# Performance work log

Hardware: AMD Instinct MI355X
Metric: run time of the kernel (lower is better)

Reference implementation:

```python
import jax, jax.numpy as jnp
import numpy as np
from jax import lax

MU = 255
H = 64            # block_hidden_size
SKIP = 256        # skip_size
NUM_LAYERS = 24
CYCLE = 6
UP_CONV = 4       # upsample_convs=[4]
UP_REPEAT = 75
LF = 80           # local_features_size
B = 2
L = 64            # local feature frames
T = L * UP_CONV * UP_REPEAT  # 19200 signal samples


def setup_inputs() -> dict:
    key = jax.random.key(0)
    ks = jax.random.split(key, 16)
    r = lambda k, shape, sc=0.05: jax.random.normal(k, shape, jnp.float32) * sc
    return {
        "local_features": jax.random.normal(ks[0], (B, L, LF), jnp.float32),
        "gold_signal": jax.random.uniform(ks[1], (B, T), jnp.float32, minval=-1.0, maxval=1.0),
        "embed_w": r(ks[2], (H, 1)),
        "embed_b": r(ks[3], (H,)),
        "up_w": r(ks[4], (LF, LF, UP_CONV)),
        "up_b": r(ks[5], (LF,)),
        "proj_w": r(ks[6], (NUM_LAYERS * 2 * H, LF)),
        "proj_b": r(ks[7], (NUM_LAYERS * 2 * H,)),
        "dil_w": r(ks[8], (NUM_LAYERS, 2 * H, H, 2)),
        "dil_b": r(ks[9], (NUM_LAYERS, 2 * H)),
        "skip_w": r(ks[10], (NUM_LAYERS, SKIP, H)),
        "skip_b": r(ks[11], (NUM_LAYERS, SKIP)),
        "res_w": r(ks[12], (NUM_LAYERS - 1, H, H)),
        "res_b": r(ks[13], (NUM_LAYERS - 1, H)),
        "out1_w": r(ks[14], (MU + 1, SKIP)),
        "out2_w": r(ks[15], (MU + 1, MU + 1)),
    }


def _causal_dilated_conv(x, w, b, dilation):
    # x: [B, C, T]; w: [O, C, 2]; left-pad so output[t] depends on inputs <= t
    xp = jnp.pad(x, ((0, 0), (0, 0), (dilation, 0)))
    y = lax.conv_general_dilated(xp, w, window_strides=(1,), padding="VALID",
                                 rhs_dilation=(dilation,),
                                 dimension_numbers=("NCH", "OIH", "NCH"))
    return y + b[None, :, None]


def _upsample(local_features, up_w, up_b, proj_w, proj_b):
    # local_features: [B, L, LF] -> cond [B, NUM_LAYERS, 2H, T]
    x = jnp.transpose(local_features, (0, 2, 1))  # [B, LF, L]
    # ConvTranspose1d with kernel_size == stride == UP_CONV (no overlap)
    y = jnp.einsum("bfl,fgk->bglk", x, up_w).reshape(x.shape[0], LF, -1)
    y = y + up_b[None, :, None]                                  # [B, LF, L*4]
    # 1x1 projection to per-layer gate conditioning (chunking in the original
    # is a memory trick, math-identical to a single conv)
    z = jnp.einsum("bft,of->bot", y, proj_w) + proj_b[None, :, None]
    z = jnp.repeat(z, UP_REPEAT, axis=-1)                        # [B, NL*2H, T]
    return z.reshape(z.shape[0], NUM_LAYERS, 2 * H, -1)


def reference(local_features, gold_signal, embed_w, embed_b, up_w, up_b,
              proj_w, proj_b, dil_w, dil_b, skip_w, skip_b, res_w, res_b,
              out1_w, out2_w):
    cond = _upsample(local_features, up_w, up_b, proj_w, proj_b)
    # embed: Conv1d(1 -> H, kernel 1)
    x = gold_signal[:, None, :] * embed_w[None, :, :] + embed_b[None, :, None]
    skip_sum = None
    for i in range(NUM_LAYERS):
        dilation = 2 ** (i % CYCLE)
        y = _causal_dilated_conv(x, dil_w[i], dil_b[i], dilation) + cond[:, i]
        gated = jnp.tanh(y[:, :H]) * jax.nn.sigmoid(y[:, H:])
        skip = jnp.einsum("bht,sh->bst", gated, skip_w[i]) + skip_b[i][None, :, None]
        skip_sum = skip if skip_sum is None else skip_sum + skip
        if i < NUM_LAYERS - 1:  # last layer has no residual out_conv
            x = x + jnp.einsum("bht,oh->bot", gated, res_w[i]) + res_b[i][None, :, None]
    h = jnp.einsum("bst,os->bot", jax.nn.relu(skip_sum), out1_w)
    h = jnp.einsum("bst,os->bot", jax.nn.relu(h), out2_w)
    return jax.nn.log_softmax(h, axis=1)  # [B, MU+1, T]
```

## Files before the change

kernel.cpp:

```cpp
#include <hip/hip_runtime.h>
#include <math.h>

#define T_TOT 19200
#define HD    64
#define SKIPN 256
#define NLAYER 24
#define LFN   80
#define NB    2
#define NTL   128
#define HALO  64
#define XR    (NTL + HALO)
#define NGT   (T_TOT / NTL)
#define NOH   64
#define NTH   (T_TOT / NOH)

typedef float  f32x4  __attribute__((ext_vector_type(4)));
typedef __bf16 bf16x8 __attribute__((ext_vector_type(8)));
typedef __bf16 bf16x4 __attribute__((ext_vector_type(4)));

__device__ __forceinline__ f32x4 mfma16(bf16x8 a, bf16x8 b, f32x4 c) {
    return __builtin_amdgcn_mfma_f32_16x16x32_bf16(a, b, c, 0, 0, 0);
}

__global__ __launch_bounds__(256) void prep_kernel(
    const float* __restrict__ dil_w, const float* __restrict__ skip_w,
    const float* __restrict__ skip_b, const float* __restrict__ res_w,
    const float* __restrict__ out1_w, const float* __restrict__ out2_w,
    __bf16* __restrict__ A1f, __bf16* __restrict__ Asf, __bf16* __restrict__ A3f,
    __bf16* __restrict__ Ao1f, __bf16* __restrict__ Ao2f, float* __restrict__ sbsum)
{
    int idx = blockIdx.x * 256 + threadIdx.x;
    if (idx < 24 * 128 * 128) {
        {
            int j = idx & 7, lane = (idx >> 3) & 63, ks = (idx >> 9) & 3;
            int mt = (idx >> 11) & 7, l = idx >> 14;
            int row = mt * 16 + (lane & 15);
            int k   = ks * 32 + (lane >> 4) * 8 + j;
            A1f[idx] = (__bf16)dil_w[((l * 128 + row) * 64 + (k & 63)) * 2 + (k >> 6)];
        }
        {
            int j = idx & 7, lane = (idx >> 3) & 63, ks = (idx >> 9) & 1;
            int mt = (idx >> 10) & 15, l = idx >> 14;
            int row = mt * 16 + (lane & 15);
            int k   = ks * 32 + (lane >> 4) * 8 + j;
            Asf[idx] = (__bf16)skip_w[(l * 256 + row) * 64 + k];
        }
    }
    if (idx < 23 * 64 * 64) {
        int j = idx & 7, lane = (idx >> 3) & 63, ks = (idx >> 9) & 1;
        int mt = (idx >> 10) & 3, l = idx >> 12;
        int row = mt * 16 + (lane & 15);
        int k   = ks * 32 + (lane >> 4) * 8 + j;
        A3f[idx] = (__bf16)res_w[(l * 64 + row) * 64 + k];
    }
    if (idx < 256 * 256) {
        int j = idx & 7, lane = (idx >> 3) & 63, ks = (idx >> 9) & 7;
        int mt = idx >> 12;
        int row = mt * 16 + (lane & 15);
        int k   = ks * 32 + (lane >> 4) * 8 + j;
        Ao1f[idx] = (__bf16)out1_w[row * 256 + k];
        Ao2f[idx] = (__bf16)out2_w[row * 256 + k];
    }
    if (idx < 256) {
        float s = 0.0f;
        #pragma unroll
        for (int l = 0; l < NLAYER; ++l) s += skip_b[l * 256 + idx];
        sbsum[idx] = s;
    }
}

__global__ __launch_bounds__(256) void up_kernel(
    const float* __restrict__ lf, const float* __restrict__ up_w,
    const float* __restrict__ up_b, float* __restrict__ y_up)
{
    int idx = blockIdx.x * 256 + threadIdx.x;
    if (idx >= NB * LFN * 256) return;
    int t4 = idx & 255;
    int g  = (idx >> 8) % LFN;
    int b  = idx / (LFN * 256);
    int l = t4 >> 2, k = t4 & 3;
    float acc = up_b[g];
    const float* lfp = lf + (b * 64 + l) * LFN;
    #pragma unroll 8
    for (int f = 0; f < LFN; ++f)
        acc += lfp[f] * up_w[(f * LFN + g) * 4 + k];
    y_up[idx] = acc;
}

__global__ __launch_bounds__(256) void proj_kernel(
    const float* __restrict__ y_up, const float* __restrict__ proj_w,
    const float* __restrict__ proj_b, float* __restrict__ z)
{
    int idx = blockIdx.x * 256 + threadIdx.x;
    if (idx >= NB * 3072 * 256) return;
    int t4 = idx & 255;
    int o  = (idx >> 8) % 3072;
    int b  = idx / (3072 * 256);
    float acc = proj_b[o];
    const float* yp = y_up + b * LFN * 256 + t4;
    const float* wp = proj_w + o * LFN;
    #pragma unroll 8
    for (int g = 0; g < LFN; ++g)
        acc += wp[g] * yp[g * 256];
    z[idx] = acc;
}

__global__ __launch_bounds__(256, 2) void layer_group(
    const float* __restrict__ gold, const float* __restrict__ ew,
    const float* __restrict__ eb,
    const __bf16* __restrict__ xg_in, __bf16* __restrict__ xg_out,
    const float* __restrict__ zbuf, const float* __restrict__ dil_b,
    const float* __restrict__ res_b,
    const __bf16* __restrict__ A1f, const __bf16* __restrict__ A3f,
    __bf16* __restrict__ G, int L0, int first, int last)
{
    __shared__ __bf16 xh[XR][72];
    __shared__ __bf16 Gs[XR][72];
    __shared__ float  zs[4][128];

    const int b    = blockIdx.y;
    const int t0   = blockIdx.x * NTL;
    const int tid  = threadIdx.x;
    const int lane = tid & 63;
    const int w    = tid >> 6;
    const int n16  = lane & 15;
    const int quad = lane >> 4;
    const int q0   = ((t0 - HALO > 0) ? t0 - HALO : 0) / 75;

    bf16x8 z8;
    #pragma unroll
    for (int u = 0; u < 8; ++u) z8[u] = (__bf16)0.0f;

    if (first) {
        for (int idx = tid; idx < XR * 8; idx += 256) {
            int r = idx >> 3, hc = (idx & 7) * 8;
            int t = t0 - HALO + r;
            bf16x8 v = z8;
            if (t >= 0) {
                float gv = gold[b * T_TOT + t];
                #pragma unroll
                for (int u = 0; u < 8; ++u)
                    v[u] = (__bf16)(gv * ew[hc + u] + eb[hc + u]);
            }
            *(bf16x8*)&xh[r][hc] = v;
        }
    } else {
        for (int idx = tid; idx < XR * 8; idx += 256) {
            int r = idx >> 3, hc = (idx & 7) * 8;
            int t = t0 - HALO + r;
            bf16x8 v = (t >= 0)
                ? *(const bf16x8*)&xg_in[((size_t)b * T_TOT + t) * 64 + hc] : z8;
            *(bf16x8*)&xh[r][hc] = v;
        }
    }

    const bf16x8* A1v = (const bf16x8*)A1f;
    const bf16x8* A3v = (const bf16x8*)A3f;
    f32x4 zero4 = {0.0f, 0.0f, 0.0f, 0.0f};

    for (int j = 0; j < 6; ++j) {
        const int l = L0 + j;
        const int d = 1 << j;

        for (int idx = tid; idx < 512; idx += 256) {
            int qq = idx >> 7, o = idx & 127;
            int q = q0 + qq; if (q > 255) q = 255;
            zs[qq][o] = dil_b[l * 128 + o] +
                        zbuf[((size_t)(b * 3072 + l * 128 + o)) * 256 + q];
        }
        bf16x8 a1a[4], a1b[4];
        #pragma unroll
        for (int ks = 0; ks < 4; ++ks) {
            a1a[ks] = A1v[((l * 8 + w) * 4 + ks) * 64 + lane];
            a1b[ks] = A1v[((l * 8 + 4 + w) * 4 + ks) * 64 + lane];
        }
        __syncthreads();

        #pragma unroll
        for (int nt = 0; nt < 12; ++nt) {
            int nn = nt * 16 + n16;
            int rm = (nn >= d) ? nn - d : 0;
            bf16x8 b0 = *(const bf16x8*)&xh[rm][quad * 8];
            bf16x8 b1 = *(const bf16x8*)&xh[rm][32 + quad * 8];
            bf16x8 b2 = *(const bf16x8*)&xh[nn][quad * 8];
            bf16x8 b3 = *(const bf16x8*)&xh[nn][32 + quad * 8];
            f32x4 aa = zero4, ab = zero4;
            aa = mfma16(a1a[0], b0, aa); ab = mfma16(a1b[0], b0, ab);
            aa = mfma16(a1a[1], b1, aa); ab = mfma16(a1b[1], b1, ab);
            aa = mfma16(a1a[2], b2, aa); ab = mfma16(a1b[2], b2, ab);
            aa = mfma16(a1a[3], b3, aa); ab = mfma16(a1b[3], b3, ab);

            int tt = t0 - HALO + nn;
            int qq = ((tt > 0) ? tt : 0) / 75 - q0;
            bf16x4 g4;
            #pragma unroll
            for (int r = 0; r < 4; ++r) {
                int o = w * 16 + quad * 4 + r;
                float ya = aa[r] + zs[qq][o];
                float yb = ab[r] + zs[qq][o + 64];
                float th = 1.0f - 2.0f * __builtin_amdgcn_rcpf(__expf(2.0f * ya) + 1.0f);
                float sg = __builtin_amdgcn_rcpf(1.0f + __expf(-yb));
                g4[r] = (__bf16)(th * sg);
            }
            *(bf16x4*)&Gs[nn][w * 16 + quad * 4] = g4;
        }
        __syncthreads();

        __bf16* Gl = G + (((size_t)l * NB + b) * T_TOT + t0) * 64;
        for (int idx = tid; idx < 128 * 8; idx += 256) {
            int rr = idx >> 3, hc = (idx & 7) * 8;
            *(bf16x8*)&Gl[rr * 64 + hc] = *(const bf16x8*)&Gs[HALO + rr][hc];
        }

        if (l < NLAYER - 1) {
            bf16x8 a3[2];
            #pragma unroll
            for (int ks = 0; ks < 2; ++ks)
                a3[ks] = A3v[((l * 4 + w) * 2 + ks) * 64 + lane];
            int o0 = w * 16 + quad * 4;
            f32x4 rb = *(const f32x4*)&res_b[l * 64 + o0];
            #pragma unroll
            for (int nt = 0; nt < 12; ++nt) {
                int nn = nt * 16 + n16;
                bf16x8 g0 = *(const bf16x8*)&Gs[nn][quad * 8];
                bf16x8 g1 = *(const bf16x8*)&Gs[nn][32 + quad * 8];
                f32x4 ar = zero4;
                ar = mfma16(a3[0], g0, ar);
                ar = mfma16(a3[1], g1, ar);
                bf16x4 xo = *(const bf16x4*)&xh[nn][o0];
                bf16x4 xn;
                #pragma unroll
                for (int r = 0; r < 4; ++r)
                    xn[r] = (__bf16)((float)xo[r] + ar[r] + rb[r]);
                *(bf16x4*)&xh[nn][o0] = xn;
            }
        }
    }

    if (!last) {
        __syncthreads();
        for (int idx = tid; idx < 128 * 8; idx += 256) {
            int rr = idx >> 3, hc = (idx & 7) * 8;
            *(bf16x8*)&xg_out[((size_t)b * T_TOT + t0 + rr) * 64 + hc] =
                *(const bf16x8*)&xh[HALO + rr][hc];
        }
    }
}

__global__ __launch_bounds__(256, 4) void head_mfma(
    const __bf16* __restrict__ G, const __bf16* __restrict__ Asf,
    const float* __restrict__ sbsum, const __bf16* __restrict__ Ao1f,
    const __bf16* __restrict__ Ao2f, float* __restrict__ out)
{
    __shared__ __bf16 Vs[NOH][264];
    __shared__ float redm[4][4][16];
    __shared__ float reds[4][4][16];

    const int b    = blockIdx.y;
    const int t0   = blockIdx.x * NOH;
    const int tid  = threadIdx.x;
    const int lane = tid & 63;
    const int w    = tid >> 6;
    const int n16  = lane & 15;
    const int quad = lane >> 4;

    f32x4 zero4 = {0.0f, 0.0f, 0.0f, 0.0f};
    f32x4 acc[4][4];
    #pragma unroll
    for (int mt = 0; mt < 4; ++mt)
        #pragma unroll
        for (int nt = 0; nt < 4; ++nt) acc[mt][nt] = zero4;

    const bf16x8* Asv = (const bf16x8*)Asf;

    for (int l = 0; l < NLAYER; ++l) {
        const __bf16* Gl = G + (((size_t)l * NB + b) * T_TOT + t0) * 64;
        #pragma unroll
        for (int ks = 0; ks < 2; ++ks) {
            bf16x8 bfr[4];
            #pragma unroll
            for (int nt = 0; nt < 4; ++nt)
                bfr[nt] = *(const bf16x8*)&Gl[(nt * 16 + n16) * 64 + ks * 32 + quad * 8];
            #pragma unroll
            for (int mt = 0; mt < 4; ++mt) {
                bf16x8 af = Asv[((l * 16 + w * 4 + mt) * 2 + ks) * 64 + lane];
                #pragma unroll
                for (int nt = 0; nt < 4; ++nt)
                    acc[mt][nt] = mfma16(af, bfr[nt], acc[mt][nt]);
            }
        }
    }
    {
        int s0 = w * 64 + quad * 4;
        #pragma unroll
        for (int mt = 0; mt < 4; ++mt) {
            #pragma unroll
            for (int nt = 0; nt < 4; ++nt) {
                bf16x4 v4;
                #pragma unroll
                for (int r = 0; r < 4; ++r)
                    v4[r] = (__bf16)fmaxf(acc[mt][nt][r] + sbsum[s0 + mt * 16 + r], 0.0f);
                *(bf16x4*)&Vs[nt * 16 + n16][s0 + mt * 16] = v4;
            }
        }
    }
    __syncthreads();

    const bf16x8* W1v = (const bf16x8*)Ao1f;
    const bf16x8* W2v = (const bf16x8*)Ao2f;

    #pragma unroll
    for (int mt = 0; mt < 4; ++mt)
        #pragma unroll
        for (int nt = 0; nt < 4; ++nt) acc[mt][nt] = zero4;
    #pragma unroll
    for (int ks = 0; ks < 8; ++ks) {
        bf16x8 bfr[4];
        #pragma unroll
        for (int nt = 0; nt < 4; ++nt)
            bfr[nt] = *(const bf16x8*)&Vs[nt * 16 + n16][ks * 32 + quad * 8];
        #pragma unroll
        for (int mt = 0; mt < 4; ++mt) {
            bf16x8 af = W1v[((w * 4 + mt) * 8 + ks) * 64 + lane];
            #pragma unroll
            for (int nt = 0; nt < 4; ++nt)
                acc[mt][nt] = mfma16(af, bfr[nt], acc[mt][nt]);
        }
    }
    __syncthreads();
    #pragma unroll
    for (int mt = 0; mt < 4; ++mt)
        #pragma unroll
        for (int nt = 0; nt < 4; ++nt) {
            int o0 = w * 64 + mt * 16 + quad * 4;
            bf16x4 v4;
            #pragma unroll
            for (int r = 0; r < 4; ++r)
                v4[r] = (__bf16)fmaxf(acc[mt][nt][r], 0.0f);
            *(bf16x4*)&Vs[nt * 16 + n16][o0] = v4;
        }
    __syncthreads();

    #pragma unroll
    for (int mt = 0; mt < 4; ++mt)
        #pragma unroll
        for (int nt = 0; nt < 4; ++nt) acc[mt][nt] = zero4;
    #pragma unroll
    for (int ks = 0; ks < 8; ++ks) {
        bf16x8 bfr[4];
        #pragma unroll
        for (int nt = 0; nt < 4; ++nt)
            bfr[nt] = *(const bf16x8*)&Vs[nt * 16 + n16][ks * 32 + quad * 8];
        #pragma unroll
        for (int mt = 0; mt < 4; ++mt) {
            bf16x8 af = W2v[((w * 4 + mt) * 8 + ks) * 64 + lane];
            #pragma unroll
            for (int nt = 0; nt < 4; ++nt)
                acc[mt][nt] = mfma16(af, bfr[nt], acc[mt][nt]);
        }
    }

    float lmax[4], lsum[4];
    #pragma unroll
    for (int nt = 0; nt < 4; ++nt) {
        float m = -1e30f;
        #pragma unroll
        for (int mt = 0; mt < 4; ++mt)
            #pragma unroll
            for (int r = 0; r < 4; ++r) m = fmaxf(m, acc[mt][nt][r]);
        m = fmaxf(m, __shfl_xor(m, 16, 64));
        m = fmaxf(m, __shfl_xor(m, 32, 64));
        lmax[nt] = m;
    }
    if (quad == 0) {
        #pragma unroll
        for (int nt = 0; nt < 4; ++nt) redm[w][nt][n16] = lmax[nt];
    }
    __syncthreads();
    #pragma unroll
    for (int nt = 0; nt < 4; ++nt) {
        float m = redm[0][nt][n16];
        m = fmaxf(m, redm[1][nt][n16]);
        m = fmaxf(m, redm[2][nt][n16]);
        m = fmaxf(m, redm[3][nt][n16]);
        lmax[nt] = m;
        float s = 0.0f;
        #pragma unroll
        for (int mt = 0; mt < 4; ++mt)
            #pragma unroll
            for (int r = 0; r < 4; ++r) s += __expf(acc[mt][nt][r] - m);
        s += __shfl_xor(s, 16, 64);
        s += __shfl_xor(s, 32, 64);
        lsum[nt] = s;
    }
    if (quad == 0) {
        #pragma unroll
        for (int nt = 0; nt < 4; ++nt) reds[w][nt][n16] = lsum[nt];
    }
    __syncthreads();
    #pragma unroll
    for (int nt = 0; nt < 4; ++nt) {
        float s = reds[0][nt][n16] + reds[1][nt][n16] +
                  reds[2][nt][n16] + reds[3][nt][n16];
        float lse = lmax[nt] + logf(s);
        int t = t0 + nt * 16 + n16;
        #pragma unroll
        for (int mt = 0; mt < 4; ++mt)
            #pragma unroll
            for (int r = 0; r < 4; ++r) {
                int o = w * 64 + mt * 16 + quad * 4 + r;
                out[((size_t)(b * SKIPN + o)) * T_TOT + t] = acc[mt][nt][r] - lse;
            }
    }
}

extern "C" void kernel_launch(void* const* d_in, const int* in_sizes, int n_in,
                              void* d_out, int out_size, void* d_ws, size_t ws_size,
                              hipStream_t stream) {
    const float* lf       = (const float*)d_in[0];
    const float* gold     = (const float*)d_in[1];
    const float* embed_w  = (const float*)d_in[2];
    const float* embed_b  = (const float*)d_in[3];
    const float* up_w     = (const float*)d_in[4];
    const float* up_b     = (const float*)d_in[5];
    const float* proj_w   = (const float*)d_in[6];
    const float* proj_b   = (const float*)d_in[7];
    const float* dil_w    = (const float*)d_in[8];
    const float* dil_b    = (const float*)d_in[9];
    const float* skip_w   = (const float*)d_in[10];
    const float* skip_b   = (const float*)d_in[11];
    const float* res_w    = (const float*)d_in[12];
    const float* res_b    = (const float*)d_in[13];
    const float* out1_w   = (const float*)d_in[14];
    const float* out2_w   = (const float*)d_in[15];

    __bf16* A1f  = (__bf16*)d_ws;
    __bf16* Asf  = A1f + 393216;
    __bf16* A3f  = Asf + 393216;
    __bf16* Ao1f = A3f + 94208;
    __bf16* Ao2f = Ao1f + 65536;
    __bf16* G    = Ao2f + 65536;
    __bf16* xga  = G + (size_t)NLAYER * NB * T_TOT * HD;
    __bf16* xgb  = xga + (size_t)NB * T_TOT * HD;
    float*  sbsum = (float*)(xgb + (size_t)NB * T_TOT * HD);
    float*  y_up  = sbsum + 256;
    float*  zbuf  = y_up + NB * LFN * 256;

    prep_kernel<<<(24 * 128 * 128 + 255) / 256, 256, 0, stream>>>(
        dil_w, skip_w, skip_b, res_w, out1_w, out2_w,
        A1f, Asf, A3f, Ao1f, Ao2f, sbsum);
    up_kernel  <<<(NB * LFN * 256 + 255) / 256, 256, 0, stream>>>(lf, up_w, up_b, y_up);
    proj_kernel<<<(NB * 3072 * 256) / 256,      256, 0, stream>>>(y_up, proj_w, proj_b, zbuf);

    const __bf16* xin[4] = { xga, xga, xgb, xga };
    __bf16*       xout[4] = { xga, xgb, xga, xgb };
    for (int g = 0; g < 4; ++g) {
        layer_group<<<dim3(NGT, NB), 256, 0, stream>>>(
            gold, embed_w, embed_b, xin[g], xout[g],
            zbuf, dil_b, res_b, A1f, A3f, G,
            6 * g, (g == 0) ? 1 : 0, (g == 3) ? 1 : 0);
    }

    head_mfma<<<dim3(NTH, NB), 256, 0, stream>>>(G, Asf, sbsum, Ao1f, Ao2f, (float*)d_out);
}
```

Measured before the change: 408.3 us.

## Double layer_group waves, chunk G layout per time tile, halve head tile

The layer kernel now runs 512 threads per block, with two wave groups each covering half of the 12 time subtiles, which doubles parallelism over the 300 blocks. The gated activation buffer G is relaid out so that each 32-sample chunk holds all 24 layers contiguously, which gives the head kernel locality across layers. The head kernel's time tile shrinks from 64 to 32 samples, doubling its grid for better CU occupancy at the cost of reloading the weights twice as often. Register pressure under launch_bounds(512,4) may force spills.

New measurement: 382.5 us. -6.3%, faster.

```diff
diff --git a/kernel.cpp b/kernel.cpp
--- a/kernel.cpp
+++ b/kernel.cpp
@@ -11,8 +11,9 @@
 #define HALO  64
 #define XR    (NTL + HALO)
 #define NGT   (T_TOT / NTL)
-#define NOH   64
+#define NOH   32
 #define NTH   (T_TOT / NOH)
+#define NCH   (T_TOT / 32)
 
 typedef float  f32x4  __attribute__((ext_vector_type(4)));
 typedef __bf16 bf16x8 __attribute__((ext_vector_type(8)));
@@ -105,7 +106,7 @@
     z[idx] = acc;
 }
 
-__global__ __launch_bounds__(256, 2) void layer_group(
+__global__ __launch_bounds__(512, 4) void layer_group(
     const float* __restrict__ gold, const float* __restrict__ ew,
     const float* __restrict__ eb,
     const __bf16* __restrict__ xg_in, __bf16* __restrict__ xg_out,
@@ -119,10 +120,13 @@
     __shared__ float  zs[4][128];
 
     const int b    = blockIdx.y;
-    const int t0   = blockIdx.x * NTL;
+    const int tb   = blockIdx.x;
+    const int t0   = tb * NTL;
     const int tid  = threadIdx.x;
     const int lane = tid & 63;
     const int w    = tid >> 6;
+    const int wm   = w & 3;
+    const int wg   = w >> 2;
     const int n16  = lane & 15;
     const int quad = lane >> 4;
     const int q0   = ((t0 - HALO > 0) ? t0 - HALO : 0) / 75;
@@ -132,7 +136,7 @@
     for (int u = 0; u < 8; ++u) z8[u] = (__bf16)0.0f;
 
     if (first) {
-        for (int idx = tid; idx < XR * 8; idx += 256) {
+        for (int idx = tid; idx < XR * 8; idx += 512) {
             int r = idx >> 3, hc = (idx & 7) * 8;
             int t = t0 - HALO + r;
             bf16x8 v = z8;
@@ -145,7 +149,7 @@
             *(bf16x8*)&xh[r][hc] = v;
         }
     } else {
-        for (int idx = tid; idx < XR * 8; idx += 256) {
+        for (int idx = tid; idx < XR * 8; idx += 512) {
             int r = idx >> 3, hc = (idx & 7) * 8;
             int t = t0 - HALO + r;
             bf16x8 v = (t >= 0)
@@ -162,8 +166,8 @@
         const int l = L0 + j;
         const int d = 1 << j;
 
-        for (int idx = tid; idx < 512; idx += 256) {
-            int qq = idx >> 7, o = idx & 127;
+        if (tid < 512) {
+            int qq = tid >> 7, o = tid & 127;
             int q = q0 + qq; if (q > 255) q = 255;
             zs[qq][o] = dil_b[l * 128 + o] +
                         zbuf[((size_t)(b * 3072 + l * 128 + o)) * 256 + q];
@@ -171,13 +175,14 @@
         bf16x8 a1a[4], a1b[4];
         #pragma unroll
         for (int ks = 0; ks < 4; ++ks) {
-            a1a[ks] = A1v[((l * 8 + w) * 4 + ks) * 64 + lane];
-            a1b[ks] = A1v[((l * 8 + 4 + w) * 4 + ks) * 64 + lane];
+            a1a[ks] = A1v[((l * 8 + wm) * 4 + ks) * 64 + lane];
+            a1b[ks] = A1v[((l * 8 + 4 + wm) * 4 + ks) * 64 + lane];
         }
         __syncthreads();
 
         #pragma unroll
-        for (int nt = 0; nt < 12; ++nt) {
+        for (int nt0 = 0; nt0 < 6; ++nt0) {
+            int nt = wg * 6 + nt0;
             int nn = nt * 16 + n16;
             int rm = (nn >= d) ? nn - d : 0;
             bf16x8 b0 = *(const bf16x8*)&xh[rm][quad * 8];
@@ -195,33 +200,36 @@
             bf16x4 g4;
             #pragma unroll
             for (int r = 0; r < 4; ++r) {
-                int o = w * 16 + quad * 4 + r;
+                int o = wm * 16 + quad * 4 + r;
                 float ya = aa[r] + zs[qq][o];
                 float yb = ab[r] + zs[qq][o + 64];
                 float th = 1.0f - 2.0f * __builtin_amdgcn_rcpf(__expf(2.0f * ya) + 1.0f);
                 float sg = __builtin_amdgcn_rcpf(1.0f + __expf(-yb));
                 g4[r] = (__bf16)(th * sg);
             }
-            *(bf16x4*)&Gs[nn][w * 16 + quad * 4] = g4;
+            *(bf16x4*)&Gs[nn][wm * 16 + quad * 4] = g4;
         }
         __syncthreads();
 
-        __bf16* Gl = G + (((size_t)l * NB + b) * T_TOT + t0) * 64;
-        for (int idx = tid; idx < 128 * 8; idx += 256) {
-            int rr = idx >> 3, hc = (idx & 7) * 8;
-            *(bf16x8*)&Gl[rr * 64 + hc] = *(const bf16x8*)&Gs[HALO + rr][hc];
+        {
+            __bf16* Gl = G + (((size_t)(b * NCH + tb * 4)) * NLAYER + l) * 2048;
+            for (int idx = tid; idx < 128 * 8; idx += 512) {
+                int rr = idx >> 3, hc = (idx & 7) * 8;
+                size_t off = (size_t)(rr >> 5) * (NLAYER * 2048) + (rr & 31) * 64 + hc;
+                *(bf16x8*)&Gl[off] = *(const bf16x8*)&Gs[HALO + rr][hc];
+            }
         }
 
         if (l < NLAYER - 1) {
             bf16x8 a3[2];
             #pragma unroll
             for (int ks = 0; ks < 2; ++ks)
-                a3[ks] = A3v[((l * 4 + w) * 2 + ks) * 64 + lane];
-            int o0 = w * 16 + quad * 4;
+                a3[ks] = A3v[((l * 4 + wm) * 2 + ks) * 64 + lane];
+            int o0 = wm * 16 + quad * 4;
             f32x4 rb = *(const f32x4*)&res_b[l * 64 + o0];
             #pragma unroll
-            for (int nt = 0; nt < 12; ++nt) {
-                int nn = nt * 16 + n16;
+            for (int nt0 = 0; nt0 < 6; ++nt0) {
+                int nn = (wg * 6 + nt0) * 16 + n16;
                 bf16x8 g0 = *(const bf16x8*)&Gs[nn][quad * 8];
                 bf16x8 g1 = *(const bf16x8*)&Gs[nn][32 + quad * 8];
                 f32x4 ar = zero4;
@@ -239,7 +247,7 @@
 
     if (!last) {
         __syncthreads();
-        for (int idx = tid; idx < 128 * 8; idx += 256) {
+        for (int idx = tid; idx < 128 * 8; idx += 512) {
             int rr = idx >> 3, hc = (idx & 7) * 8;
             *(bf16x8*)&xg_out[((size_t)b * T_TOT + t0 + rr) * 64 + hc] =
                 *(const bf16x8*)&xh[HALO + rr][hc];
@@ -253,11 +261,12 @@
     const __bf16* __restrict__ Ao2f, float* __restrict__ out)
 {
     __shared__ __bf16 Vs[NOH][264];
-    __shared__ float redm[4][4][16];
-    __shared__ float reds[4][4][16];
+    __shared__ float redm[4][2][16];
+    __shared__ float reds[4][2][16];
 
     const int b    = blockIdx.y;
-    const int t0   = blockIdx.x * NOH;
+    const int tcb  = blockIdx.x;
+    const int t0   = tcb * NOH;
     const int tid  = threadIdx.x;
     const int lane = tid & 63;
     const int w    = tid >> 6;
@@ -265,27 +274,28 @@
     const int quad = lane >> 4;
 
     f32x4 zero4 = {0.0f, 0.0f, 0.0f, 0.0f};
-    f32x4 acc[4][4];
+    f32x4 acc[4][2];
     #pragma unroll
     for (int mt = 0; mt < 4; ++mt)
         #pragma unroll
-        for (int nt = 0; nt < 4; ++nt) acc[mt][nt] = zero4;
+        for (int nt = 0; nt < 2; ++nt) acc[mt][nt] = zero4;
 
     const bf16x8* Asv = (const bf16x8*)Asf;
+    const __bf16* Gc  = G + ((size_t)(b * NCH + tcb)) * (NLAYER * 2048);
 
     for (int l = 0; l < NLAYER; ++l) {
-        const __bf16* Gl = G + (((size_t)l * NB + b) * T_TOT + t0) * 64;
+        const __bf16* Gl = Gc + l * 2048;
         #pragma unroll
         for (int ks = 0; ks < 2; ++ks) {
-            bf16x8 bfr[4];
-            #pragma unroll
-            for (int nt = 0; nt < 4; ++nt)
+            bf16x8 bfr[2];
+            #pragma unroll
+            for (int nt = 0; nt < 2; ++nt)
                 bfr[nt] = *(const bf16x8*)&Gl[(nt * 16 + n16) * 64 + ks * 32 + quad * 8];
             #pragma unroll
             for (int mt = 0; mt < 4; ++mt) {
                 bf16x8 af = Asv[((l * 16 + w * 4 + mt) * 2 + ks) * 64 + lane];
                 #pragma unroll
-                for (int nt = 0; nt < 4; ++nt)
+                for (int nt = 0; nt < 2; ++nt)
                     acc[mt][nt] = mfma16(af, bfr[nt], acc[mt][nt]);
             }
         }
@@ -293,16 +303,15 @@
     {
         int s0 = w * 64 + quad * 4;
         #pragma unroll
-        for (int mt = 0; mt < 4; ++mt) {
-            #pragma unroll
-            for (int nt = 0; nt < 4; ++nt) {
+        for (int mt = 0; mt < 4; ++mt)
+            #pragma unroll
+            for (int nt = 0; nt < 2; ++nt) {
                 bf16x4 v4;
                 #pragma unroll
                 for (int r = 0; r < 4; ++r)
                     v4[r] = (__bf16)fmaxf(acc[mt][nt][r] + sbsum[s0 + mt * 16 + r], 0.0f);
                 *(bf16x4*)&Vs[nt * 16 + n16][s0 + mt * 16] = v4;
             }
-        }
     }
     __syncthreads();
 
@@ -312,18 +321,18 @@
     #pragma unroll
     for (int mt = 0; mt < 4; ++mt)
         #pragma unroll
-        for (int nt = 0; nt < 4; ++nt) acc[mt][nt] = zero4;
+        for (int nt = 0; nt < 2; ++nt) acc[mt][nt] = zero4;
     #pragma unroll
     for (int ks = 0; ks < 8; ++ks) {
-        bf16x8 bfr[4];
-        #pragma unroll
-        for (int nt = 0; nt < 4; ++nt)
+        bf16x8 bfr[2];
+        #pragma unroll
+        for (int nt = 0; nt < 2; ++nt)
             bfr[nt] = *(const bf16x8*)&Vs[nt * 16 + n16][ks * 32 + quad * 8];
         #pragma unroll
         for (int mt = 0; mt < 4; ++mt) {
             bf16x8 af = W1v[((w * 4 + mt) * 8 + ks) * 64 + lane];
             #pragma unroll
-            for (int nt = 0; nt < 4; ++nt)
+            for (int nt = 0; nt < 2; ++nt)
                 acc[mt][nt] = mfma16(af, bfr[nt], acc[mt][nt]);
         }
     }
@@ -331,7 +340,7 @@
     #pragma unroll
     for (int mt = 0; mt < 4; ++mt)
         #pragma unroll
-        for (int nt = 0; nt < 4; ++nt) {
+        for (int nt = 0; nt < 2; ++nt) {
             int o0 = w * 64 + mt * 16 + quad * 4;
             bf16x4 v4;
             #pragma unroll
@@ -344,25 +353,25 @@
     #pragma unroll
     for (int mt = 0; mt < 4; ++mt)
         #pragma unroll
-        for (int nt = 0; nt < 4; ++nt) acc[mt][nt] = zero4;
+        for (int nt = 0; nt < 2; ++nt) acc[mt][nt] = zero4;
     #pragma unroll
     for (int ks = 0; ks < 8; ++ks) {
-        bf16x8 bfr[4];
-        #pragma unroll
-        for (int nt = 0; nt < 4; ++nt)
+        bf16x8 bfr[2];
+        #pragma unroll
+        for (int nt = 0; nt < 2; ++nt)
             bfr[nt] = *(const bf16x8*)&Vs[nt * 16 + n16][ks * 32 + quad * 8];
         #pragma unroll
         for (int mt = 0; mt < 4; ++mt) {
             bf16x8 af = W2v[((w * 4 + mt) * 8 + ks) * 64 + lane];
             #pragma unroll
-            for (int nt = 0; nt < 4; ++nt)
+            for (int nt = 0; nt < 2; ++nt)
                 acc[mt][nt] = mfma16(af, bfr[nt], acc[mt][nt]);
         }
     }
 
-    float lmax[4], lsum[4];
-    #pragma unroll
-    for (int nt = 0; nt < 4; ++nt) {
+    float lmax[2], lsum[2];
+    #pragma unroll
+    for (int nt = 0; nt < 2; ++nt) {
         float m = -1e30f;
         #pragma unroll
         for (int mt = 0; mt < 4; ++mt)
@@ -374,11 +383,11 @@
     }
     if (quad == 0) {
         #pragma unroll
-        for (int nt = 0; nt < 4; ++nt) redm[w][nt][n16] = lmax[nt];
+        for (int nt = 0; nt < 2; ++nt) redm[w][nt][n16] = lmax[nt];
     }
     __syncthreads();
     #pragma unroll
-    for (int nt = 0; nt < 4; ++nt) {
+    for (int nt = 0; nt < 2; ++nt) {
         float m = redm[0][nt][n16];
         m = fmaxf(m, redm[1][nt][n16]);
         m = fmaxf(m, redm[2][nt][n16]);
@@ -395,11 +404,11 @@
     }
     if (quad == 0) {
         #pragma unroll
-        for (int nt = 0; nt < 4; ++nt) reds[w][nt][n16] = lsum[nt];
+        for (int nt = 0; nt < 2; ++nt) reds[w][nt][n16] = lsum[nt];
     }
     __syncthreads();
     #pragma unroll
-    for (int nt = 0; nt < 4; ++nt) {
+    for (int nt = 0; nt < 2; ++nt) {
         float s = reds[0][nt][n16] + reds[1][nt][n16] +
                   reds[2][nt][n16] + reds[3][nt][n16];
         float lse = lmax[nt] + logf(s);
@@ -440,7 +449,7 @@
     __bf16* Ao1f = A3f + 94208;
     __bf16* Ao2f = Ao1f + 65536;
     __bf16* G    = Ao2f + 65536;
-    __bf16* xga  = G + (size_t)NLAYER * NB * T_TOT * HD;
+    __bf16* xga  = G + (size_t)NB * NCH * NLAYER * 2048;
     __bf16* xgb  = xga + (size_t)NB * T_TOT * HD;
     float*  sbsum = (float*)(xgb + (size_t)NB * T_TOT * HD);
     float*  y_up  = sbsum + 256;
@@ -455,7 +464,7 @@
     const __bf16* xin[4] = { xga, xga, xgb, xga };
     __bf16*       xout[4] = { xga, xgb, xga, xgb };
     for (int g = 0; g < 4; ++g) {
-        layer_group<<<dim3(NGT, NB), 256, 0, stream>>>(
+        layer_group<<<dim3(NGT, NB), 512, 0, stream>>>(
             gold, embed_w, embed_b, xin[g], xout[g],
             zbuf, dil_b, res_b, A1f, A3f, G,
             6 * g, (g == 0) ? 1 : 0, (g == 3) ? 1 : 0);
```
